# Performance work log

Measured on AMD Instinct MI355X. Metric: run time of the kernel, lower is better.

## Reference

```python
import jax, jax.numpy as jnp
import numpy as np

N_NODES = 50000


def _gcn_conv_mean(x, W, src, dst, deg, dinv_sqrt):
    # GCNConv math: h = x @ W; message = dinv[src]*dinv[dst] * h[src];
    # aggr='mean' -> scatter-sum into dst then divide by in-degree (incl. self loop).
    h = x @ W                                   # [N, outdim]
    norm = dinv_sqrt[src] * dinv_sqrt[dst]      # [E+N]
    msg = norm[:, None] * h[src]                # gather + scale
    agg = jax.ops.segment_sum(msg, dst, num_segments=N_NODES)
    return agg / deg[:, None]                   # mean aggregation (deg >= 1 via self loops)


def setup_inputs() -> dict:
    key = jax.random.key(0)
    k1, k2, k3, k4 = jax.random.split(key, 4)
    x = jax.random.normal(k1, (N_NODES, 64), dtype=jnp.float32)
    edge_index = jax.random.randint(k2, (2, 1600000), 0, N_NODES, dtype=jnp.int64)
    scale = 1.0 / np.sqrt(64.0)
    W1 = jax.random.normal(k3, (64, 64), dtype=jnp.float32) * scale
    W2 = jax.random.normal(k4, (64, 64), dtype=jnp.float32) * scale
    return {"x": x, "edge_index": edge_index, "W1": W1, "W2": W2}


def reference(x, edge_index, W1, W2):
    # add self loops (add_self_loops=True, improved=False -> fill value 1)
    loop = jnp.arange(N_NODES, dtype=edge_index.dtype)
    src = jnp.concatenate([edge_index[0], loop])
    dst = jnp.concatenate([edge_index[1], loop])
    # degree over destination with unit edge weights (gcn_norm)
    deg = jax.ops.segment_sum(jnp.ones_like(src, dtype=x.dtype), dst, num_segments=N_NODES)
    dinv_sqrt = jnp.where(deg > 0, jax.lax.rsqrt(jnp.maximum(deg, 1e-12)), 0.0)
    x1 = jax.nn.relu(_gcn_conv_mean(x, W1, src, dst, deg, dinv_sqrt))
    x2 = jax.nn.sigmoid(_gcn_conv_mean(x, W2, src, dst, deg, dinv_sqrt))
    return x1 * x2
```

## Files before the change

### kernel.cpp

```cpp
#include <hip/hip_runtime.h>

#define NFEAT 64
#define BNODES 64
#define MAXBUCK 1024
#define SORT_LDS 6144
#define KPT 4

__device__ __forceinline__ unsigned short f2bf(float f) {
    unsigned int u = __float_as_uint(f);
    return (unsigned short)((u + 0x7FFFu + ((u >> 16) & 1u)) >> 16);
}
__device__ __forceinline__ float bf2f(unsigned short h) {
    return __uint_as_float(((unsigned int)h) << 16);
}

__global__ void k_zero(int* __restrict__ p, int n) {
    for (int i = threadIdx.x; i < n; i += 1024) p[i] = 0;
}

__global__ __launch_bounds__(256) void k_histb(
        const int* __restrict__ ei, int* __restrict__ bcnt, int E, int nb) {
    __shared__ int h[MAXBUCK];
    __shared__ int s_not64;
    if (threadIdx.x == 0) s_not64 = 0;
    for (int i = threadIdx.x; i < nb; i += 256) h[i] = 0;
    __syncthreads();
    if (ei[2 * threadIdx.x + 1] != 0) s_not64 = 1;
    __syncthreads();
    int is64 = s_not64 ? 0 : 1;
    int per = (E + gridDim.x - 1) / gridDim.x;
    int e0 = blockIdx.x * per;
    int e1 = min(e0 + per, E);
    if (is64) {
        const int2* d64 = (const int2*)ei + E;
        for (int i = e0 + threadIdx.x; i < e1; i += 256)
            atomicAdd(&h[d64[i].x >> 6], 1);
    } else {
        for (int i = e0 + threadIdx.x; i < e1; i += 256)
            atomicAdd(&h[ei[E + i] >> 6], 1);
    }
    __syncthreads();
    for (int i = threadIdx.x; i < nb; i += 256)
        if (h[i]) atomicAdd(&bcnt[i], h[i]);
}

__global__ void k_bscan(const int* __restrict__ bcnt, int* __restrict__ bstart,
                        int* __restrict__ bfill, int nb, int E) {
    __shared__ int s[1024];
    int t = threadIdx.x;
    int mine = (t < nb) ? bcnt[t] : 0;
    s[t] = mine;
    __syncthreads();
    for (int off = 1; off < 1024; off <<= 1) {
        int v = (t >= off) ? s[t - off] : 0;
        __syncthreads();
        s[t] += v;
        __syncthreads();
    }
    if (t < nb) {
        int excl = s[t] - mine;
        bstart[t] = excl;
        bfill[t] = excl;
    }
    if (t == 0) bstart[nb] = E;
}

__global__ __launch_bounds__(1024) void k_part(
        const int* __restrict__ ei, int* __restrict__ bfill,
        unsigned int* __restrict__ edges, int E, int nb) {
    __shared__ int h[MAXBUCK];
    __shared__ int chunk[MAXBUCK];
    __shared__ int cur[MAXBUCK];
    __shared__ int s_not64;
    if (threadIdx.x == 0) s_not64 = 0;
    for (int i = threadIdx.x; i < nb; i += 1024) h[i] = 0;
    __syncthreads();
    if (threadIdx.x < 256 && ei[2 * threadIdx.x + 1] != 0) s_not64 = 1;
    __syncthreads();
    int is64 = s_not64 ? 0 : 1;
    int per = (E + gridDim.x - 1) / gridDim.x;
    int e0 = blockIdx.x * per;
    int e1 = min(e0 + per, E);

    unsigned int ed[KPT];
    if (is64) {
        const int2* s64 = (const int2*)ei;
        const int2* d64 = s64 + E;
#pragma unroll
        for (int k = 0; k < KPT; ++k) {
            int i = e0 + threadIdx.x + k * 1024;
            if (i < e1) {
                unsigned int s = (unsigned int)s64[i].x;
                unsigned int d = (unsigned int)d64[i].x;
                ed[k] = (d << 16) | s;
                atomicAdd(&h[d >> 6], 1);
            }
        }
    } else {
#pragma unroll
        for (int k = 0; k < KPT; ++k) {
            int i = e0 + threadIdx.x + k * 1024;
            if (i < e1) {
                unsigned int s = (unsigned int)ei[i];
                unsigned int d = (unsigned int)ei[E + i];
                ed[k] = (d << 16) | s;
                atomicAdd(&h[d >> 6], 1);
            }
        }
    }
    __syncthreads();
    for (int i = threadIdx.x; i < nb; i += 1024) {
        int c = h[i];
        chunk[i] = c ? atomicAdd(&bfill[i], c) : 0;
        cur[i] = 0;
    }
    __syncthreads();
#pragma unroll
    for (int k = 0; k < KPT; ++k) {
        int i = e0 + threadIdx.x + k * 1024;
        if (i < e1) {
            int b = (int)(ed[k] >> 22);
            int r = atomicAdd(&cur[b], 1);
            edges[chunk[b] + r] = ed[k];
        }
    }
}

template <bool INPLACE>
__global__ __launch_bounds__(256) void k_sort3(
        const unsigned int* __restrict__ edges, const int* __restrict__ bstart,
        const float* __restrict__ x, int* __restrict__ count,
        int* __restrict__ ptr, float* __restrict__ scale,
        unsigned short* __restrict__ y, unsigned short* __restrict__ sorted_src,
        int N, int E) {
    __shared__ int cnt64[BNODES];
    __shared__ int pos64[BNODES];
    __shared__ unsigned int raw[INPLACE ? SORT_LDS : 1];
    int tid = threadIdx.x;
    int vbase = blockIdx.x * BNODES;
    int es = bstart[blockIdx.x];
    int ee = bstart[blockIdx.x + 1];
    int m = ee - es;
    if (tid < BNODES) cnt64[tid] = 0;
    __syncthreads();

    if (INPLACE) {
        int mm = min(m, SORT_LDS);
        for (int i = tid; i < mm; i += 256) {
            unsigned int e = edges[es + i];
            raw[i] = e;
            atomicAdd(&cnt64[(e >> 16) & 63u], 1);
        }
        for (int i = SORT_LDS + tid; i < m; i += 256)
            atomicAdd(&cnt64[(edges[es + i] >> 16) & 63u], 1);
    } else {
        for (int i = tid; i < m; i += 256)
            atomicAdd(&cnt64[(edges[es + i] >> 16) & 63u], 1);
    }
    __syncthreads();

    if (tid < BNODES) {
        int c = cnt64[tid];
        int inc = c;
#pragma unroll
        for (int d = 1; d < 64; d <<= 1) {
            int t2 = __shfl_up(inc, d, 64);
            if (tid >= d) inc += t2;
        }
        int off = inc - c;
        pos64[tid] = es + off;
        int v = vbase + tid;
        if (v < N) {
            count[v] = c;
            ptr[v] = es + off;
            float dg = (float)(c + 1);
            scale[v] = rsqrtf(dg) / dg;
        }
    }
    __syncthreads();

    if (INPLACE) {
        int mm = min(m, SORT_LDS);
        for (int i = tid; i < mm; i += 256) {
            unsigned int e = raw[i];
            int p = atomicAdd(&pos64[(e >> 16) & 63u], 1);
            sorted_src[p] = (unsigned short)(e & 0xFFFFu);
        }
        for (int i = SORT_LDS + tid; i < m; i += 256) {
            unsigned int e = edges[es + i];
            int p = atomicAdd(&pos64[(e >> 16) & 63u], 1);
            sorted_src[p] = (unsigned short)(e & 0xFFFFu);
        }
    } else {
        for (int i = tid; i < m; i += 256) {
            unsigned int e = edges[es + i];
            int p = atomicAdd(&pos64[(e >> 16) & 63u], 1);
            sorted_src[p] = (unsigned short)(e & 0xFFFFu);
        }
    }

    const float4* x4 = (const float4*)x;
    for (int i = tid; i < BNODES * 16; i += 256) {
        int r = i >> 4, j = i & 15;
        int v = vbase + r;
        if (v < N) {
            float dg = (float)(cnt64[r] + 1);
            float dv = rsqrtf(dg);
            float4 q = x4[(size_t)v * 16 + j];
            ushort4 o;
            o.x = f2bf(q.x * dv); o.y = f2bf(q.y * dv);
            o.z = f2bf(q.z * dv); o.w = f2bf(q.w * dv);
            ((ushort4*)y)[(size_t)v * 16 + j] = o;
        }
    }
}

__global__ __launch_bounds__(256) void k_gather(
        const unsigned short* __restrict__ y, const float* __restrict__ scale,
        const int* __restrict__ ptr, const int* __restrict__ count,
        const unsigned short* __restrict__ sorted_src,
        float* __restrict__ agg_out, int N) {
    int wave = threadIdx.x >> 6;
    int lane = threadIdx.x & 63;
    int vbase = blockIdx.x * 16 + wave * 4;

    for (int vi = 0; vi < 4; ++vi) {
        int v = vbase + vi;
        if (v >= N) return;
        int start = ptr[v];
        int cnt = count[v];
        float sc = scale[v];
        float a0 = bf2f(y[(size_t)v * NFEAT + lane]);
        float a1 = 0.f, a2 = 0.f, a3 = 0.f, a4 = 0.f, a5 = 0.f, a6 = 0.f, a7 = 0.f;

        for (int c = 0; c < cnt; c += 64) {
            int m = min(64, cnt - c);
            int s_l = 0;
            if (lane < m) s_l = (int)sorted_src[start + c + lane];
            int j = 0;
            for (; j + 8 <= m; j += 8) {
                int s0 = __shfl(s_l, j + 0, 64), s1 = __shfl(s_l, j + 1, 64);
                int s2 = __shfl(s_l, j + 2, 64), s3 = __shfl(s_l, j + 3, 64);
                int s4 = __shfl(s_l, j + 4, 64), s5 = __shfl(s_l, j + 5, 64);
                int s6 = __shfl(s_l, j + 6, 64), s7 = __shfl(s_l, j + 7, 64);
                a0 += bf2f(y[(size_t)s0 * NFEAT + lane]);
                a1 += bf2f(y[(size_t)s1 * NFEAT + lane]);
                a2 += bf2f(y[(size_t)s2 * NFEAT + lane]);
                a3 += bf2f(y[(size_t)s3 * NFEAT + lane]);
                a4 += bf2f(y[(size_t)s4 * NFEAT + lane]);
                a5 += bf2f(y[(size_t)s5 * NFEAT + lane]);
                a6 += bf2f(y[(size_t)s6 * NFEAT + lane]);
                a7 += bf2f(y[(size_t)s7 * NFEAT + lane]);
            }
            for (; j < m; ++j) {
                int s0 = __shfl(s_l, j, 64);
                a0 += bf2f(y[(size_t)s0 * NFEAT + lane]);
            }
        }
        float a = ((a0 + a1) + (a2 + a3)) + ((a4 + a5) + (a6 + a7));
        agg_out[(size_t)v * NFEAT + lane] = a * sc;
    }
}

__global__ __launch_bounds__(256) void k_epi6(
        const float* __restrict__ agg, const float* __restrict__ W1,
        const float* __restrict__ W2, float* __restrict__ out, int N) {
    __shared__ float at[64 * 65];
    int tid = threadIdx.x;
    int lane = tid & 63;
    int v0 = blockIdx.x * 64;

    const float4* agg4 = (const float4*)agg;
    for (int i = tid; i < 64 * 16; i += 256) {
        int v = i >> 4, j = i & 15;
        float4 q;
        if (v0 + v < N) q = agg4[(size_t)(v0 + v) * 16 + j];
        else { q.x = q.y = q.z = q.w = 0.f; }
        float* r = &at[v * 65 + j * 4];
        r[0] = q.x; r[1] = q.y; r[2] = q.z; r[3] = q.w;
    }
    __syncthreads();

    int cb = __builtin_amdgcn_readfirstlane((tid >> 6) * 16);
    float acc1[16], acc2[16];
#pragma unroll
    for (int c = 0; c < 16; ++c) { acc1[c] = 0.f; acc2[c] = 0.f; }

    for (int k = 0; k < NFEAT; ++k) {
        float ak = at[lane * 65 + k];
        const float* w1k = W1 + (size_t)k * NFEAT + cb;
        const float* w2k = W2 + (size_t)k * NFEAT + cb;
#pragma unroll
        for (int c = 0; c < 16; ++c) {
            acc1[c] = fmaf(ak, w1k[c], acc1[c]);
            acc2[c] = fmaf(ak, w2k[c], acc2[c]);
        }
    }

    int v = v0 + lane;
    if (v < N) {
        float4* o4 = (float4*)(out + (size_t)v * NFEAT + cb);
#pragma unroll
        for (int g = 0; g < 4; ++g) {
            float4 q;
            float r0 = fmaxf(acc1[4 * g + 0], 0.f), s0 = 1.f / (1.f + __expf(-acc2[4 * g + 0]));
            float r1 = fmaxf(acc1[4 * g + 1], 0.f), s1 = 1.f / (1.f + __expf(-acc2[4 * g + 1]));
            float r2 = fmaxf(acc1[4 * g + 2], 0.f), s2 = 1.f / (1.f + __expf(-acc2[4 * g + 2]));
            float r3 = fmaxf(acc1[4 * g + 3], 0.f), s3 = 1.f / (1.f + __expf(-acc2[4 * g + 3]));
            q.x = r0 * s0; q.y = r1 * s1; q.z = r2 * s2; q.w = r3 * s3;
            o4[g] = q;
        }
    }
}

extern "C" void kernel_launch(void* const* d_in, const int* in_sizes, int n_in,
                              void* d_out, int out_size, void* d_ws, size_t ws_size,
                              hipStream_t stream) {
    const float* x  = (const float*)d_in[0];
    const int*   ei = (const int*)d_in[1];
    const float* W1 = (const float*)d_in[2];
    const float* W2 = (const float*)d_in[3];
    float* out = (float*)d_out;

    const int N = in_sizes[0] / NFEAT;
    const int E = in_sizes[1] / 2;
    const int nb = (N + BNODES - 1) / BNODES;

    char* ws = (char*)d_ws;
    size_t off = 0;
    auto alloc = [&](size_t bytes) {
        char* p = ws + off;
        off = (off + bytes + 255) & ~(size_t)255;
        return p;
    };
    int*   count  = (int*)alloc((size_t)N * 4);
    float* scale  = (float*)alloc((size_t)N * 4);
    int*   ptr    = (int*)alloc((size_t)N * 4);
    int*   bcnt   = (int*)alloc((size_t)MAXBUCK * 4);
    int*   bstart = (int*)alloc((size_t)(MAXBUCK + 1) * 4);
    int*   bfill  = (int*)alloc((size_t)MAXBUCK * 4);

    size_t aggB   = (size_t)N * NFEAT * 4;
    size_t edgeB  = (size_t)E * 4;
    size_t regB   = aggB > edgeB ? aggB : edgeB;
    size_t t1_need = off + regB + (size_t)N * NFEAT * 2 + (size_t)E * 2 + 1024;

    k_zero<<<1, 1024, 0, stream>>>(bcnt, MAXBUCK);
    k_histb<<<256, 256, 0, stream>>>(ei, bcnt, E, nb);
    k_bscan<<<1, 1024, 0, stream>>>(bcnt, bstart, bfill, nb, E);
    int gpart = (E + 1024 * KPT - 1) / (1024 * KPT);

    if (ws_size >= t1_need) {
        char* reg = (char*)alloc(regB);
        unsigned int*   edges      = (unsigned int*)reg;
        float*          agg        = (float*)reg;
        unsigned short* y          = (unsigned short*)alloc((size_t)N * NFEAT * 2);
        unsigned short* sorted_src = (unsigned short*)alloc((size_t)E * 2);

        k_part<<<gpart, 1024, 0, stream>>>(ei, bfill, edges, E, nb);
        k_sort3<false><<<nb, 256, 0, stream>>>(edges, bstart, x, count, ptr,
                                               scale, y, sorted_src, N, E);
        k_gather<<<(N + 15) / 16, 256, 0, stream>>>(y, scale, ptr, count,
                                                    sorted_src, agg, N);
        k_epi6<<<(N + 63) / 64, 256, 0, stream>>>(agg, W1, W2, out, N);
    } else {
        unsigned int*   edges = (unsigned int*)alloc(edgeB);
        unsigned short* y     = (unsigned short*)alloc((size_t)N * NFEAT * 2);
        unsigned short* sorted_src;
        bool inplace;
        if (ws_size >= off + (size_t)E * 2) {
            sorted_src = (unsigned short*)alloc((size_t)E * 2);
            inplace = false;
        } else {
            sorted_src = (unsigned short*)edges;
            inplace = true;
        }
        k_part<<<gpart, 1024, 0, stream>>>(ei, bfill, edges, E, nb);
        if (inplace) {
            k_sort3<true><<<nb, 256, 0, stream>>>(edges, bstart, x, count, ptr,
                                                  scale, y, sorted_src, N, E);
        } else {
            k_sort3<false><<<nb, 256, 0, stream>>>(edges, bstart, x, count, ptr,
                                                   scale, y, sorted_src, N, E);
        }
        k_gather<<<(N + 15) / 16, 256, 0, stream>>>(y, scale, ptr, count,
                                                    sorted_src, out, N);
        k_epi6<<<(N + 63) / 64, 256, 0, stream>>>(out, W1, W2, out, N);
    }
}
```

Before: 114.7 us.

## Split bf16 feature table into two column halves and gather each in separate pass

The sorted-feature write now stores y as two planes of 32 bf16 columns each instead of one 64-wide row layout. The gather kernel becomes two launches, one per half, and each wave processes two edges at once (32 lanes per edge). The half-warps' partial sums are combined with a cross-lane shuffle. The aim is to shrink the randomly accessed working set per pass (each plane is half the size) so more of it stays in cache. The cost is reading the edge lists twice, an extra launch, and 64-byte row reads instead of 128-byte ones.

Measured after the change: 148.1 us. 29.1% more time.

```diff
diff --git a/kernel.cpp b/kernel.cpp
--- a/kernel.cpp
+++ b/kernel.cpp
@@ -210,18 +210,21 @@
             ushort4 o;
             o.x = f2bf(q.x * dv); o.y = f2bf(q.y * dv);
             o.z = f2bf(q.z * dv); o.w = f2bf(q.w * dv);
-            ((ushort4*)y)[(size_t)v * 16 + j] = o;
-        }
-    }
-}
-
-__global__ __launch_bounds__(256) void k_gather(
-        const unsigned short* __restrict__ y, const float* __restrict__ scale,
+            int hpl = j >> 3, jj = j & 7;
+            ((ushort4*)(y + (size_t)hpl * N * 32))[(size_t)v * 8 + jj] = o;
+        }
+    }
+}
+
+__global__ __launch_bounds__(256) void k_gather2(
+        const unsigned short* __restrict__ yh, const float* __restrict__ scale,
         const int* __restrict__ ptr, const int* __restrict__ count,
         const unsigned short* __restrict__ sorted_src,
-        float* __restrict__ agg_out, int N) {
+        float* __restrict__ agg_out, int N, int col0) {
     int wave = threadIdx.x >> 6;
     int lane = threadIdx.x & 63;
+    int lo = lane & 31;
+    int hi = lane >> 5;
     int vbase = blockIdx.x * 16 + wave * 4;
 
     for (int vi = 0; vi < 4; ++vi) {
@@ -230,7 +233,7 @@
         int start = ptr[v];
         int cnt = count[v];
         float sc = scale[v];
-        float a0 = bf2f(y[(size_t)v * NFEAT + lane]);
+        float a0 = (hi == 0) ? bf2f(yh[(size_t)v * 32 + lo]) : 0.f;
         float a1 = 0.f, a2 = 0.f, a3 = 0.f, a4 = 0.f, a5 = 0.f, a6 = 0.f, a7 = 0.f;
 
         for (int c = 0; c < cnt; c += 64) {
@@ -238,27 +241,29 @@
             int s_l = 0;
             if (lane < m) s_l = (int)sorted_src[start + c + lane];
             int j = 0;
-            for (; j + 8 <= m; j += 8) {
-                int s0 = __shfl(s_l, j + 0, 64), s1 = __shfl(s_l, j + 1, 64);
-                int s2 = __shfl(s_l, j + 2, 64), s3 = __shfl(s_l, j + 3, 64);
-                int s4 = __shfl(s_l, j + 4, 64), s5 = __shfl(s_l, j + 5, 64);
-                int s6 = __shfl(s_l, j + 6, 64), s7 = __shfl(s_l, j + 7, 64);
-                a0 += bf2f(y[(size_t)s0 * NFEAT + lane]);
-                a1 += bf2f(y[(size_t)s1 * NFEAT + lane]);
-                a2 += bf2f(y[(size_t)s2 * NFEAT + lane]);
-                a3 += bf2f(y[(size_t)s3 * NFEAT + lane]);
-                a4 += bf2f(y[(size_t)s4 * NFEAT + lane]);
-                a5 += bf2f(y[(size_t)s5 * NFEAT + lane]);
-                a6 += bf2f(y[(size_t)s6 * NFEAT + lane]);
-                a7 += bf2f(y[(size_t)s7 * NFEAT + lane]);
+            for (; j + 16 <= m; j += 16) {
+                int e0 = __shfl(s_l, j + 0 + hi, 64), e1 = __shfl(s_l, j + 2 + hi, 64);
+                int e2 = __shfl(s_l, j + 4 + hi, 64), e3 = __shfl(s_l, j + 6 + hi, 64);
+                int e4 = __shfl(s_l, j + 8 + hi, 64), e5 = __shfl(s_l, j + 10 + hi, 64);
+                int e6 = __shfl(s_l, j + 12 + hi, 64), e7 = __shfl(s_l, j + 14 + hi, 64);
+                a0 += bf2f(yh[(size_t)e0 * 32 + lo]);
+                a1 += bf2f(yh[(size_t)e1 * 32 + lo]);
+                a2 += bf2f(yh[(size_t)e2 * 32 + lo]);
+                a3 += bf2f(yh[(size_t)e3 * 32 + lo]);
+                a4 += bf2f(yh[(size_t)e4 * 32 + lo]);
+                a5 += bf2f(yh[(size_t)e5 * 32 + lo]);
+                a6 += bf2f(yh[(size_t)e6 * 32 + lo]);
+                a7 += bf2f(yh[(size_t)e7 * 32 + lo]);
             }
             for (; j < m; ++j) {
                 int s0 = __shfl(s_l, j, 64);
-                a0 += bf2f(y[(size_t)s0 * NFEAT + lane]);
+                if (hi == 0) a0 += bf2f(yh[(size_t)s0 * 32 + lo]);
             }
         }
         float a = ((a0 + a1) + (a2 + a3)) + ((a4 + a5) + (a6 + a7));
-        agg_out[(size_t)v * NFEAT + lane] = a * sc;
+        a += __shfl_xor(a, 32, 64);
+        if (hi == 0)
+            agg_out[(size_t)v * NFEAT + col0 + lo] = a * sc;
     }
 }
 
@@ -349,6 +354,7 @@
     k_histb<<<256, 256, 0, stream>>>(ei, bcnt, E, nb);
     k_bscan<<<1, 1024, 0, stream>>>(bcnt, bstart, bfill, nb, E);
     int gpart = (E + 1024 * KPT - 1) / (1024 * KPT);
+    int gblk = (N + 15) / 16;
 
     if (ws_size >= t1_need) {
         char* reg = (char*)alloc(regB);
@@ -360,8 +366,10 @@
         k_part<<<gpart, 1024, 0, stream>>>(ei, bfill, edges, E, nb);
         k_sort3<false><<<nb, 256, 0, stream>>>(edges, bstart, x, count, ptr,
                                                scale, y, sorted_src, N, E);
-        k_gather<<<(N + 15) / 16, 256, 0, stream>>>(y, scale, ptr, count,
-                                                    sorted_src, agg, N);
+        k_gather2<<<gblk, 256, 0, stream>>>(y, scale, ptr, count,
+                                            sorted_src, agg, N, 0);
+        k_gather2<<<gblk, 256, 0, stream>>>(y + (size_t)N * 32, scale, ptr, count,
+                                            sorted_src, agg, N, 32);
         k_epi6<<<(N + 63) / 64, 256, 0, stream>>>(agg, W1, W2, out, N);
     } else {
         unsigned int*   edges = (unsigned int*)alloc(edgeB);
@@ -383,8 +391,10 @@
             k_sort3<false><<<nb, 256, 0, stream>>>(edges, bstart, x, count, ptr,
                                                    scale, y, sorted_src, N, E);
         }
-        k_gather<<<(N + 15) / 16, 256, 0, stream>>>(y, scale, ptr, count,
-                                                    sorted_src, out, N);
+        k_gather2<<<gblk, 256, 0, stream>>>(y, scale, ptr, count,
+                                            sorted_src, out, N, 0);
+        k_gather2<<<gblk, 256, 0, stream>>>(y + (size_t)N * 32, scale, ptr, count,
+                                            sorted_src, out, N, 32);
         k_epi6<<<(N + 63) / 64, 256, 0, stream>>>(out, W1, W2, out, N);
     }
 }
```

## Fuse histogram, bucket scan and partition into one cooperative kernel

Applied to the files above, without the earlier changes.

Merges the separate bucket histogram, prefix scan and partition kernels into one cooperative launch that uses grid-wide syncs. Each block's per-bucket histogram of its own edges is reused for partitioning, so the second pass over the destination indices and two kernel launches go away. The risk is that a cooperative launch requires every block to be resident at once: with E=1.6M and 4096 edges per block this is about 391 blocks of 1024 threads, and a grid that large may exceed co-residency limits and fail to launch. Grid syncs also add their own latency.

Measured after the change: 191.5 us. 67.0% more time.

```diff
diff --git a/kernel.cpp b/kernel.cpp
--- a/kernel.cpp
+++ b/kernel.cpp
@@ -1,4 +1,5 @@
 #include <hip/hip_runtime.h>
+#include <hip/hip_cooperative_groups.h>
 
 #define NFEAT 64
 #define BNODES 64
@@ -6,6 +7,8 @@
 #define SORT_LDS 6144
 #define KPT 4
 
+namespace cg = cooperative_groups;
+
 __device__ __forceinline__ unsigned short f2bf(float f) {
     unsigned int u = __float_as_uint(f);
     return (unsigned short)((u + 0x7FFFu + ((u >> 16) & 1u)) >> 16);
@@ -18,66 +21,23 @@
     for (int i = threadIdx.x; i < n; i += 1024) p[i] = 0;
 }
 
-__global__ __launch_bounds__(256) void k_histb(
-        const int* __restrict__ ei, int* __restrict__ bcnt, int E, int nb) {
-    __shared__ int h[MAXBUCK];
-    __shared__ int s_not64;
-    if (threadIdx.x == 0) s_not64 = 0;
-    for (int i = threadIdx.x; i < nb; i += 256) h[i] = 0;
-    __syncthreads();
-    if (ei[2 * threadIdx.x + 1] != 0) s_not64 = 1;
-    __syncthreads();
-    int is64 = s_not64 ? 0 : 1;
-    int per = (E + gridDim.x - 1) / gridDim.x;
-    int e0 = blockIdx.x * per;
-    int e1 = min(e0 + per, E);
-    if (is64) {
-        const int2* d64 = (const int2*)ei + E;
-        for (int i = e0 + threadIdx.x; i < e1; i += 256)
-            atomicAdd(&h[d64[i].x >> 6], 1);
-    } else {
-        for (int i = e0 + threadIdx.x; i < e1; i += 256)
-            atomicAdd(&h[ei[E + i] >> 6], 1);
-    }
-    __syncthreads();
-    for (int i = threadIdx.x; i < nb; i += 256)
-        if (h[i]) atomicAdd(&bcnt[i], h[i]);
-}
-
-__global__ void k_bscan(const int* __restrict__ bcnt, int* __restrict__ bstart,
-                        int* __restrict__ bfill, int nb, int E) {
-    __shared__ int s[1024];
-    int t = threadIdx.x;
-    int mine = (t < nb) ? bcnt[t] : 0;
-    s[t] = mine;
-    __syncthreads();
-    for (int off = 1; off < 1024; off <<= 1) {
-        int v = (t >= off) ? s[t - off] : 0;
-        __syncthreads();
-        s[t] += v;
-        __syncthreads();
-    }
-    if (t < nb) {
-        int excl = s[t] - mine;
-        bstart[t] = excl;
-        bfill[t] = excl;
-    }
-    if (t == 0) bstart[nb] = E;
-}
-
-__global__ __launch_bounds__(1024) void k_part(
-        const int* __restrict__ ei, int* __restrict__ bfill,
+__global__ __launch_bounds__(1024) void k_build(
+        const int* __restrict__ ei, int* __restrict__ bcnt,
+        int* __restrict__ bstart, int* __restrict__ bfill,
         unsigned int* __restrict__ edges, int E, int nb) {
+    cg::grid_group grid = cg::this_grid();
     __shared__ int h[MAXBUCK];
     __shared__ int chunk[MAXBUCK];
     __shared__ int cur[MAXBUCK];
     __shared__ int s_not64;
+
     if (threadIdx.x == 0) s_not64 = 0;
     for (int i = threadIdx.x; i < nb; i += 1024) h[i] = 0;
     __syncthreads();
     if (threadIdx.x < 256 && ei[2 * threadIdx.x + 1] != 0) s_not64 = 1;
     __syncthreads();
     int is64 = s_not64 ? 0 : 1;
+
     int per = (E + gridDim.x - 1) / gridDim.x;
     int e0 = blockIdx.x * per;
     int e1 = min(e0 + per, E);
@@ -109,6 +69,33 @@
         }
     }
     __syncthreads();
+    for (int i = threadIdx.x; i < nb; i += 1024)
+        if (h[i]) atomicAdd(&bcnt[i], h[i]);
+
+    grid.sync();
+
+    if (blockIdx.x == 0) {
+        __shared__ int s[1024];
+        int t = threadIdx.x;
+        int mine = (t < nb) ? bcnt[t] : 0;
+        s[t] = mine;
+        __syncthreads();
+        for (int off = 1; off < 1024; off <<= 1) {
+            int v = (t >= off) ? s[t - off] : 0;
+            __syncthreads();
+            s[t] += v;
+            __syncthreads();
+        }
+        if (t < nb) {
+            int excl = s[t] - mine;
+            bstart[t] = excl;
+            bfill[t] = excl;
+        }
+        if (t == 0) bstart[nb] = E;
+    }
+
+    grid.sync();
+
     for (int i = threadIdx.x; i < nb; i += 1024) {
         int c = h[i];
         chunk[i] = c ? atomicAdd(&bfill[i], c) : 0;
@@ -346,9 +333,8 @@
     size_t t1_need = off + regB + (size_t)N * NFEAT * 2 + (size_t)E * 2 + 1024;
 
     k_zero<<<1, 1024, 0, stream>>>(bcnt, MAXBUCK);
-    k_histb<<<256, 256, 0, stream>>>(ei, bcnt, E, nb);
-    k_bscan<<<1, 1024, 0, stream>>>(bcnt, bstart, bfill, nb, E);
     int gpart = (E + 1024 * KPT - 1) / (1024 * KPT);
+    int gblk = (N + 15) / 16;
 
     if (ws_size >= t1_need) {
         char* reg = (char*)alloc(regB);
@@ -357,11 +343,14 @@
         unsigned short* y          = (unsigned short*)alloc((size_t)N * NFEAT * 2);
         unsigned short* sorted_src = (unsigned short*)alloc((size_t)E * 2);
 
-        k_part<<<gpart, 1024, 0, stream>>>(ei, bfill, edges, E, nb);
+        void* bargs[] = {(void*)&ei, (void*)&bcnt, (void*)&bstart, (void*)&bfill,
+                         (void*)&edges, (void*)&E, (void*)&nb};
+        hipLaunchCooperativeKernel((void*)k_build, dim3(gpart), dim3(1024),
+                                   bargs, 0, stream);
         k_sort3<false><<<nb, 256, 0, stream>>>(edges, bstart, x, count, ptr,
                                                scale, y, sorted_src, N, E);
-        k_gather<<<(N + 15) / 16, 256, 0, stream>>>(y, scale, ptr, count,
-                                                    sorted_src, agg, N);
+        k_gather<<<gblk, 256, 0, stream>>>(y, scale, ptr, count,
+                                           sorted_src, agg, N);
         k_epi6<<<(N + 63) / 64, 256, 0, stream>>>(agg, W1, W2, out, N);
     } else {
         unsigned int*   edges = (unsigned int*)alloc(edgeB);
@@ -375,7 +364,10 @@
             sorted_src = (unsigned short*)edges;
             inplace = true;
         }
-        k_part<<<gpart, 1024, 0, stream>>>(ei, bfill, edges, E, nb);
+        void* bargs[] = {(void*)&ei, (void*)&bcnt, (void*)&bstart, (void*)&bfill,
+                         (void*)&edges, (void*)&E, (void*)&nb};
+        hipLaunchCooperativeKernel((void*)k_build, dim3(gpart), dim3(1024),
+                                   bargs, 0, stream);
         if (inplace) {
             k_sort3<true><<<nb, 256, 0, stream>>>(edges, bstart, x, count, ptr,
                                                   scale, y, sorted_src, N, E);
@@ -383,8 +375,8 @@
             k_sort3<false><<<nb, 256, 0, stream>>>(edges, bstart, x, count, ptr,
                                                    scale, y, sorted_src, N, E);
         }
-        k_gather<<<(N + 15) / 16, 256, 0, stream>>>(y, scale, ptr, count,
-                                                    sorted_src, out, N);
+        k_gather<<<gblk, 256, 0, stream>>>(y, scale, ptr, count,
+                                           sorted_src, out, N);
         k_epi6<<<(N + 63) / 64, 256, 0, stream>>>(out, W1, W2, out, N);
     }
 }
```
